# Kernel optimization log

Measured on AMD Instinct MI355X. Metric: run time of the kernel, lower is better.

## Reference

```python
import jax, jax.numpy as jnp
import numpy as np

W_BIT = 4
HALF = 2 ** (W_BIT - 1)  # 8: recentering offset used in post_init
GROUP_SIZE = 128
IN_FEATURES = 4096
OUT_FEATURES = 11008
TOKENS = 32


def setup_inputs() -> dict:
    key = jax.random.key(0)
    k1, k2, k3, k4, k5 = jax.random.split(key, 5)
    n_groups = IN_FEATURES // GROUP_SIZE
    x = jax.random.normal(k1, (TOKENS, IN_FEATURES), dtype=jnp.float32)
    # unpacked 4-bit weight codes in [0, 15]
    qweight = jax.random.randint(k2, (IN_FEATURES, OUT_FEATURES), 0, 2 ** W_BIT, dtype=jnp.int32)
    # group-wise 4-bit zero-point codes in [0, 15]
    qzeros = jax.random.randint(k3, (n_groups, OUT_FEATURES), 0, 2 ** W_BIT, dtype=jnp.int32)
    # group-wise scales (positive, small, like real quant scales)
    scales = jax.random.uniform(k4, (n_groups, OUT_FEATURES), dtype=jnp.float32, minval=0.001, maxval=0.02)
    bias = jax.random.normal(k5, (OUT_FEATURES,), dtype=jnp.float32)
    return {"x": x, "qweight": qweight, "qzeros": qzeros, "scales": scales, "bias": bias}


def reference(x, qweight, qzeros, scales, bias):
    # post_init recenters codes: q -> q - 2^(b-1), z -> z - 2^(b-1)
    w_int = (qweight - HALF).astype(jnp.float32)            # [K, N]
    z_int = (qzeros - HALF).astype(jnp.float32)             # [K//gs, N]
    # broadcast group-wise zeros/scales along K
    z_rep = jnp.repeat(z_int, GROUP_SIZE, axis=0)           # [K, N]
    s_rep = jnp.repeat(scales, GROUP_SIZE, axis=0)          # [K, N]
    # fused dequant-GEMM: y = x @ ((q - z) * s) + bias
    w_deq = (w_int - z_rep) * s_rep                         # [K, N] fp32
    out = x @ w_deq + bias                                  # [T, N]
    return out
```

## Files before the change

kernel.cpp:

```cpp
#include <hip/hip_runtime.h>
#include <hip/hip_bf16.h>


#define TOKENS   32
#define KDIM     4096
#define NDIM     11008
#define GS       128
#define KSPLIT   8
#define KCHUNK   512
#define BLOCK    256
#define BLOCK_N  128

typedef __attribute__((ext_vector_type(8))) _Float16 half8;
typedef __attribute__((ext_vector_type(4))) float   floatx4;

__global__ __launch_bounds__(256) void awq_cvt_kernel(
    const float* __restrict__ x, unsigned short* __restrict__ xh)
{
    const int i = blockIdx.x * 256 + threadIdx.x;
    const float4 v = ((const float4*)x)[i];
    ushort4 o;
    o.x = __builtin_bit_cast(unsigned short, (_Float16)v.x);
    o.y = __builtin_bit_cast(unsigned short, (_Float16)v.y);
    o.z = __builtin_bit_cast(unsigned short, (_Float16)v.z);
    o.w = __builtin_bit_cast(unsigned short, (_Float16)v.w);
    ((ushort4*)xh)[i] = o;
}

__global__ __launch_bounds__(256) void awq_init_kernel(
    const float* __restrict__ bias, float* __restrict__ out)
{
    const int n = blockIdx.x * 256 + threadIdx.x;
    out[blockIdx.y * NDIM + n] = bias[n];
}

template<bool ATOMIC>
__global__ __launch_bounds__(BLOCK) void awq_gemm_mfma(
    const unsigned short* __restrict__ xh,
    const int*   __restrict__ qw,
    const int*   __restrict__ qz,
    const float* __restrict__ sc,
    float*       __restrict__ dst)
{
    const int tid  = threadIdx.x;
    const int lane = tid & 63;
    const int wv   = tid >> 6;
    const int wv_n = wv & 1;
    const int wv_k = wv >> 1;
    const int col  = lane & 15;
    const int quad = lane >> 4;
    const int nb   = blockIdx.x * BLOCK_N + wv_n * 64;
    const int nc   = nb + 4 * col;

    __shared__ float4 red[2 * 64 * 8];

    floatx4 acc[4][2];
    #pragma unroll
    for (int nt = 0; nt < 4; ++nt) {
        acc[nt][0] = (floatx4){0.f, 0.f, 0.f, 0.f};
        acc[nt][1] = (floatx4){0.f, 0.f, 0.f, 0.f};
    }

    for (int gi = 0; gi < KCHUNK / GS / 2; ++gi) {
        const int g   = blockIdx.y * (KCHUNK / GS) + wv_k * (KCHUNK / GS / 2) + gi;
        const int kc0 = g * GS;

        float s[4], nzs[4];
        #pragma unroll
        for (int nt = 0; nt < 4; ++nt) {
            const int n  = nc + nt;
            const float sv = sc[(size_t)g * NDIM + n];
            const int   zv = qz[(size_t)g * NDIM + n];
            s[nt] = sv; nzs[nt] = -(float)zv * sv;
        }

        const int* qbase = qw + (size_t)(kc0 + quad * 8) * NDIM + nc;
        const unsigned short* xr0 = xh + (size_t)col * KDIM + kc0 + quad * 8;
        const unsigned short* xr1 = xr0 + 16 * KDIM;

        #pragma unroll 2
        for (int ks = 0; ks < GS / 32; ++ks) {
            int4 q[8];
            #pragma unroll
            for (int j = 0; j < 8; ++j)
                q[j] = *(const int4*)(qbase + (size_t)(ks * 32 + j) * NDIM);

            const half8 a0 = *(const half8*)(xr0 + ks * 32);
            const half8 a1 = *(const half8*)(xr1 + ks * 32);

            half8 b0, b1, b2, b3;
            #pragma unroll
            for (int j = 0; j < 8; ++j) {
                b0[j] = (_Float16)fmaf((float)q[j].x, s[0], nzs[0]);
                b1[j] = (_Float16)fmaf((float)q[j].y, s[1], nzs[1]);
                b2[j] = (_Float16)fmaf((float)q[j].z, s[2], nzs[2]);
                b3[j] = (_Float16)fmaf((float)q[j].w, s[3], nzs[3]);
            }
            acc[0][0] = __builtin_amdgcn_mfma_f32_16x16x32_f16(a0, b0, acc[0][0], 0, 0, 0);
            acc[0][1] = __builtin_amdgcn_mfma_f32_16x16x32_f16(a1, b0, acc[0][1], 0, 0, 0);
            acc[1][0] = __builtin_amdgcn_mfma_f32_16x16x32_f16(a0, b1, acc[1][0], 0, 0, 0);
            acc[1][1] = __builtin_amdgcn_mfma_f32_16x16x32_f16(a1, b1, acc[1][1], 0, 0, 0);
            acc[2][0] = __builtin_amdgcn_mfma_f32_16x16x32_f16(a0, b2, acc[2][0], 0, 0, 0);
            acc[2][1] = __builtin_amdgcn_mfma_f32_16x16x32_f16(a1, b2, acc[2][1], 0, 0, 0);
            acc[3][0] = __builtin_amdgcn_mfma_f32_16x16x32_f16(a0, b3, acc[3][0], 0, 0, 0);
            acc[3][1] = __builtin_amdgcn_mfma_f32_16x16x32_f16(a1, b3, acc[3][1], 0, 0, 0);
        }
    }

    if (wv_k == 1) {
        float4* rp = red + (size_t)(wv_n * 64 + lane) * 8;
        #pragma unroll
        for (int nt = 0; nt < 4; ++nt)
            #pragma unroll
            for (int h = 0; h < 2; ++h) {
                const int js = ((nt * 2 + h) + (lane & 7)) & 7;
                rp[js] = make_float4(acc[nt][h][0], acc[nt][h][1],
                                     acc[nt][h][2], acc[nt][h][3]);
            }
    }
    __syncthreads();
    if (wv_k != 0) return;
    {
        const float4* rp = red + (size_t)(wv_n * 64 + lane) * 8;
        #pragma unroll
        for (int nt = 0; nt < 4; ++nt)
            #pragma unroll
            for (int h = 0; h < 2; ++h) {
                const int js = ((nt * 2 + h) + (lane & 7)) & 7;
                const float4 v = rp[js];
                acc[nt][h][0] += v.x; acc[nt][h][1] += v.y;
                acc[nt][h][2] += v.z; acc[nt][h][3] += v.w;
            }
    }

    if (ATOMIC) {
        #pragma unroll
        for (int h = 0; h < 2; ++h)
            #pragma unroll
            for (int r = 0; r < 4; ++r) {
                float* pp = dst + (size_t)(h * 16 + quad * 4 + r) * NDIM + nc;
                unsafeAtomicAdd(pp + 0, acc[0][h][r]);
                unsafeAtomicAdd(pp + 1, acc[1][h][r]);
                unsafeAtomicAdd(pp + 2, acc[2][h][r]);
                unsafeAtomicAdd(pp + 3, acc[3][h][r]);
            }
    } else {
        float* pbase = dst + (size_t)blockIdx.y * TOKENS * NDIM;
        #pragma unroll
        for (int h = 0; h < 2; ++h)
            #pragma unroll
            for (int r = 0; r < 4; ++r) {
                const float4 v = make_float4(acc[0][h][r], acc[1][h][r],
                                             acc[2][h][r], acc[3][h][r]);
                *(float4*)(pbase + (size_t)(h * 16 + quad * 4 + r) * NDIM + nc) = v;
            }
    }
}

__global__ __launch_bounds__(256) void awq_reduce_kernel(
    const float* __restrict__ part,
    const float* __restrict__ bias,
    float*       __restrict__ out)
{
    const int o = blockIdx.x * 256 + threadIdx.x;
    const int t = o / (NDIM / 4);
    const int c = o - t * (NDIM / 4);
    const float4* p4 = (const float4*)part;
    float4 sum = ((const float4*)bias)[c];
    #pragma unroll
    for (int s = 0; s < KSPLIT; ++s) {
        const float4 v = p4[(size_t)(s * TOKENS + t) * (NDIM / 4) + c];
        sum.x += v.x; sum.y += v.y; sum.z += v.z; sum.w += v.w;
    }
    ((float4*)out)[o] = sum;
}

extern "C" void kernel_launch(void* const* d_in, const int* in_sizes, int n_in,
                              void* d_out, int out_size, void* d_ws, size_t ws_size,
                              hipStream_t stream) {
    const float* x    = (const float*)d_in[0];
    const int*   qw   = (const int*)  d_in[1];
    const int*   qz   = (const int*)  d_in[2];
    const float* sc   = (const float*)d_in[3];
    const float* bias = (const float*)d_in[4];
    float* out = (float*)d_out;

    const size_t xh_bytes   = 512 * 1024;
    const size_t part_bytes = (size_t)KSPLIT * TOKENS * NDIM * sizeof(float);
    unsigned short* xh = (unsigned short*)d_ws;
    float* part = (float*)((char*)d_ws + xh_bytes);

    awq_cvt_kernel<<<(TOKENS * KDIM / 4) / 256, 256, 0, stream>>>(x, xh);

    if (ws_size >= xh_bytes + part_bytes) {
        awq_gemm_mfma<false><<<dim3(NDIM / BLOCK_N, KSPLIT), BLOCK, 0, stream>>>(
            xh, qw, qz, sc, part);
        awq_reduce_kernel<<<(TOKENS * NDIM / 4) / 256, 256, 0, stream>>>(
            part, bias, out);
    } else {
        awq_init_kernel<<<dim3(NDIM / 256, TOKENS), 256, 0, stream>>>(bias, out);
        awq_gemm_mfma<true><<<dim3(NDIM / BLOCK_N, KSPLIT), BLOCK, 0, stream>>>(
            xh, qw, qz, sc, out);
    }
}
```

Measured before the change: 266.4 us.

## Fuse x fp16 conversion into GEMM and reduce split-K with atomics

Removes the separate fp32-to-fp16 conversion kernel: the GEMM now reads fp32 activations directly and converts them in registers. It also drops the partial-buffer plus reduce-kernel path and always uses bias init followed by atomic adds into the output. This cuts two kernel launches and the partial-buffer round trip. In exchange, activation reads double in size, conversions repeat across blocks, and atomic contention on the output rises.

```diff
diff --git a/kernel.cpp b/kernel.cpp
--- a/kernel.cpp
+++ b/kernel.cpp
@@ -14,19 +14,6 @@
 typedef __attribute__((ext_vector_type(8))) _Float16 half8;
 typedef __attribute__((ext_vector_type(4))) float   floatx4;
 
-__global__ __launch_bounds__(256) void awq_cvt_kernel(
-    const float* __restrict__ x, unsigned short* __restrict__ xh)
-{
-    const int i = blockIdx.x * 256 + threadIdx.x;
-    const float4 v = ((const float4*)x)[i];
-    ushort4 o;
-    o.x = __builtin_bit_cast(unsigned short, (_Float16)v.x);
-    o.y = __builtin_bit_cast(unsigned short, (_Float16)v.y);
-    o.z = __builtin_bit_cast(unsigned short, (_Float16)v.z);
-    o.w = __builtin_bit_cast(unsigned short, (_Float16)v.w);
-    ((ushort4*)xh)[i] = o;
-}
-
 __global__ __launch_bounds__(256) void awq_init_kernel(
     const float* __restrict__ bias, float* __restrict__ out)
 {
@@ -34,9 +21,8 @@
     out[blockIdx.y * NDIM + n] = bias[n];
 }
 
-template<bool ATOMIC>
 __global__ __launch_bounds__(BLOCK) void awq_gemm_mfma(
-    const unsigned short* __restrict__ xh,
+    const float* __restrict__ x,
     const int*   __restrict__ qw,
     const int*   __restrict__ qz,
     const float* __restrict__ sc,
@@ -75,8 +61,8 @@
         }
 
         const int* qbase = qw + (size_t)(kc0 + quad * 8) * NDIM + nc;
-        const unsigned short* xr0 = xh + (size_t)col * KDIM + kc0 + quad * 8;
-        const unsigned short* xr1 = xr0 + 16 * KDIM;
+        const float* xr0 = x + (size_t)col * KDIM + kc0 + quad * 8;
+        const float* xr1 = xr0 + 16 * KDIM;
 
         #pragma unroll 2
         for (int ks = 0; ks < GS / 32; ++ks) {
@@ -85,8 +71,19 @@
             for (int j = 0; j < 8; ++j)
                 q[j] = *(const int4*)(qbase + (size_t)(ks * 32 + j) * NDIM);
 
-            const half8 a0 = *(const half8*)(xr0 + ks * 32);
-            const half8 a1 = *(const half8*)(xr1 + ks * 32);
+            const float4 af0 = *(const float4*)(xr0 + ks * 32);
+            const float4 af1 = *(const float4*)(xr0 + ks * 32 + 4);
+            const float4 ag0 = *(const float4*)(xr1 + ks * 32);
+            const float4 ag1 = *(const float4*)(xr1 + ks * 32 + 4);
+            half8 a0, a1;
+            a0[0] = (_Float16)af0.x; a0[1] = (_Float16)af0.y;
+            a0[2] = (_Float16)af0.z; a0[3] = (_Float16)af0.w;
+            a0[4] = (_Float16)af1.x; a0[5] = (_Float16)af1.y;
+            a0[6] = (_Float16)af1.z; a0[7] = (_Float16)af1.w;
+            a1[0] = (_Float16)ag0.x; a1[1] = (_Float16)ag0.y;
+            a1[2] = (_Float16)ag0.z; a1[3] = (_Float16)ag0.w;
+            a1[4] = (_Float16)ag1.x; a1[5] = (_Float16)ag1.y;
+            a1[6] = (_Float16)ag1.z; a1[7] = (_Float16)ag1.w;
 
             half8 b0, b1, b2, b3;
             #pragma unroll
@@ -133,46 +130,16 @@
             }
     }
 
-    if (ATOMIC) {
+    #pragma unroll
+    for (int h = 0; h < 2; ++h)
         #pragma unroll
-        for (int h = 0; h < 2; ++h)
-            #pragma unroll
-            for (int r = 0; r < 4; ++r) {
-                float* pp = dst + (size_t)(h * 16 + quad * 4 + r) * NDIM + nc;
-                unsafeAtomicAdd(pp + 0, acc[0][h][r]);
-                unsafeAtomicAdd(pp + 1, acc[1][h][r]);
-                unsafeAtomicAdd(pp + 2, acc[2][h][r]);
-                unsafeAtomicAdd(pp + 3, acc[3][h][r]);
-            }
-    } else {
-        float* pbase = dst + (size_t)blockIdx.y * TOKENS * NDIM;
-        #pragma unroll
-        for (int h = 0; h < 2; ++h)
-            #pragma unroll
-            for (int r = 0; r < 4; ++r) {
-                const float4 v = make_float4(acc[0][h][r], acc[1][h][r],
-                                             acc[2][h][r], acc[3][h][r]);
-                *(float4*)(pbase + (size_t)(h * 16 + quad * 4 + r) * NDIM + nc) = v;
-            }
-    }
-}
-
-__global__ __launch_bounds__(256) void awq_reduce_kernel(
-    const float* __restrict__ part,
-    const float* __restrict__ bias,
-    float*       __restrict__ out)
-{
-    const int o = blockIdx.x * 256 + threadIdx.x;
-    const int t = o / (NDIM / 4);
-    const int c = o - t * (NDIM / 4);
-    const float4* p4 = (const float4*)part;
-    float4 sum = ((const float4*)bias)[c];
-    #pragma unroll
-    for (int s = 0; s < KSPLIT; ++s) {
-        const float4 v = p4[(size_t)(s * TOKENS + t) * (NDIM / 4) + c];
-        sum.x += v.x; sum.y += v.y; sum.z += v.z; sum.w += v.w;
-    }
-    ((float4*)out)[o] = sum;
+        for (int r = 0; r < 4; ++r) {
+            float* pp = dst + (size_t)(h * 16 + quad * 4 + r) * NDIM + nc;
+            unsafeAtomicAdd(pp + 0, acc[0][h][r]);
+            unsafeAtomicAdd(pp + 1, acc[1][h][r]);
+            unsafeAtomicAdd(pp + 2, acc[2][h][r]);
+            unsafeAtomicAdd(pp + 3, acc[3][h][r]);
+        }
 }
 
 extern "C" void kernel_launch(void* const* d_in, const int* in_sizes, int n_in,
@@ -184,22 +151,9 @@
     const float* sc   = (const float*)d_in[3];
     const float* bias = (const float*)d_in[4];
     float* out = (float*)d_out;
+    (void)d_ws; (void)ws_size;
 
-    const size_t xh_bytes   = 512 * 1024;
-    const size_t part_bytes = (size_t)KSPLIT * TOKENS * NDIM * sizeof(float);
-    unsigned short* xh = (unsigned short*)d_ws;
-    float* part = (float*)((char*)d_ws + xh_bytes);
-
-    awq_cvt_kernel<<<(TOKENS * KDIM / 4) / 256, 256, 0, stream>>>(x, xh);
-
-    if (ws_size >= xh_bytes + part_bytes) {
-        awq_gemm_mfma<false><<<dim3(NDIM / BLOCK_N, KSPLIT), BLOCK, 0, stream>>>(
-            xh, qw, qz, sc, part);
-        awq_reduce_kernel<<<(TOKENS * NDIM / 4) / 256, 256, 0, stream>>>(
-            part, bias, out);
-    } else {
-        awq_init_kernel<<<dim3(NDIM / 256, TOKENS), 256, 0, stream>>>(bias, out);
-        awq_gemm_mfma<true><<<dim3(NDIM / BLOCK_N, KSPLIT), BLOCK, 0, stream>>>(
-            xh, qw, qz, sc, out);
-    }
+    awq_init_kernel<<<dim3(NDIM / 256, TOKENS), 256, 0, stream>>>(bias, out);
+    awq_gemm_mfma<<<dim3(NDIM / BLOCK_N, KSPLIT), BLOCK, 0, stream>>>(
+        x, qw, qz, sc, out);
 }
```

Measured after the change: 276.2 us. +3.7%, slower.
